# Performance work log

Measured on AMD Instinct MI355X. Metric: run time of the kernel, lower is better.

Reference implementation:

```python
import jax, jax.numpy as jnp
import numpy as np

D_MODEL = 1024
NUM_HEADS = 16
HEAD_DIM = D_MODEL // NUM_HEADS


def setup_inputs() -> dict:
    key = jax.random.key(0)
    k_x, k_wqkv, k_bqkv, k_wfc, k_bfc = jax.random.split(key, 5)
    scale_in = 1.0 / np.sqrt(D_MODEL)
    return {
        "x": jax.random.normal(k_x, (2, 2048, D_MODEL), dtype=jnp.float32),
        # torch nn.Linear stores weight as [out_features, in_features]
        "w_qkv": jax.random.uniform(k_wqkv, (3 * D_MODEL, D_MODEL), jnp.float32, -scale_in, scale_in),
        "b_qkv": jax.random.uniform(k_bqkv, (3 * D_MODEL,), jnp.float32, -scale_in, scale_in),
        "w_fc": jax.random.uniform(k_wfc, (D_MODEL, D_MODEL), jnp.float32, -scale_in, scale_in),
        "b_fc": jax.random.uniform(k_bfc, (D_MODEL,), jnp.float32, -scale_in, scale_in),
    }


def reference(x, w_qkv, b_qkv, w_fc, b_fc):
    B, S, _ = x.shape
    # fused QKV projection: [B,S,3*d_model]
    qkv = jnp.einsum("bsd,ed->bse", x, w_qkv) + b_qkv
    # [B,S,H,3*head_dim] -> [B,H,S,3*head_dim]
    qkv = qkv.reshape(B, S, NUM_HEADS, 3 * HEAD_DIM).transpose(0, 2, 1, 3)
    Q, K, V = jnp.split(qkv, 3, axis=-1)  # each [B,H,S,head_dim]
    scores = jnp.einsum("bhqd,bhkd->bhqk", Q, K) / np.sqrt(HEAD_DIM).astype(np.float32)
    attention = jax.nn.softmax(scores, axis=-1)  # [B,H,S,S]
    values = jnp.einsum("bhqk,bhkd->bhqd", attention, V)
    # [B,H,S,head_dim] -> [B,S,d_model]
    values = values.transpose(0, 2, 1, 3).reshape(B, S, D_MODEL)
    out = jnp.einsum("bsd,ed->bse", values, w_fc) + b_fc
    return out
```

## Files before the change

### kernel.cpp

```cpp
#include <hip/hip_runtime.h>
#include <hip/hip_bf16.h>

#define D_MODEL 1024
#define NH 16
#define HD 64
#define BATCH 2
#define SEQ 2048

typedef __attribute__((ext_vector_type(8))) short short8;
typedef __attribute__((ext_vector_type(4))) float floatx4;

static __device__ __forceinline__ short f2bf(float f) {
    __hip_bfloat16 h = __float2bfloat16(f);
    return *reinterpret_cast<short*>(&h);
}
static __device__ __forceinline__ unsigned int pk2bf(float a, float b) {
    float2 t; t.x = a; t.y = b;
    __hip_bfloat162 h2 = __float22bfloat162_rn(t);
    return *reinterpret_cast<unsigned int*>(&h2);
}

__global__ __launch_bounds__(256) void cvt_all(
    const float* __restrict__ x, const float* __restrict__ wq,
    const float* __restrict__ wf,
    short* __restrict__ Xb, short* __restrict__ Wqb, short* __restrict__ Wfb)
{
    int i = blockIdx.x * 256 + threadIdx.x;
    const float* src; short* dst; int off;
    if (i < 524288)      { src = x;  dst = Xb;  off = i; }
    else if (i < 917504) { src = wq; dst = Wqb; off = i - 524288; }
    else                 { src = wf; dst = Wfb; off = i - 917504; }
    float4 a = *reinterpret_cast<const float4*>(src + off * 8);
    float4 b = *reinterpret_cast<const float4*>(src + off * 8 + 4);
    short8 o;
    o[0] = f2bf(a.x); o[1] = f2bf(a.y); o[2] = f2bf(a.z); o[3] = f2bf(a.w);
    o[4] = f2bf(b.x); o[5] = f2bf(b.y); o[6] = f2bf(b.z); o[7] = f2bf(b.w);
    *reinterpret_cast<short8*>(dst + off * 8) = o;
}

__global__ __launch_bounds__(256) void qkv_gemm(
    const short* __restrict__ X, const short* __restrict__ W,
    const float* __restrict__ bias,
    short* __restrict__ Qs, short* __restrict__ Ks, short* __restrict__ Vt_g)
{
    __shared__ __align__(16) short As[128][72];
    __shared__ __align__(16) short Bs[64][72];
    const int tid = threadIdx.x;
    const int bx = blockIdx.x;
    const int m0 = blockIdx.y * 128;
    const int n0 = bx * 64;
    const int h = bx / 3, t = bx % 3;
    const int bi = m0 >> 11;
    const int sl0 = m0 & 2047;
    const int w = tid >> 6, lane = tid & 63;
    const int quad = lane >> 4, l15 = lane & 15;
    const int wm2 = w >> 1, wn2 = w & 1;

    floatx4 acc[4][2];
#pragma unroll
    for (int i = 0; i < 4; i++)
#pragma unroll
        for (int j = 0; j < 2; j++) acc[i][j] = (floatx4)0.0f;

    for (int k0 = 0; k0 < 1024; k0 += 64) {
        __syncthreads();
#pragma unroll
        for (int i = 0; i < 4; i++) {
            int c = tid + i * 256;
            int row = c >> 3, ck = c & 7;
            *reinterpret_cast<uint4*>(&As[row][ck * 8]) =
                *reinterpret_cast<const uint4*>(&X[(m0 + row) * 1024 + k0 + ck * 8]);
        }
#pragma unroll
        for (int i = 0; i < 2; i++) {
            int c = tid + i * 256;
            int row = c >> 3, ck = c & 7;
            *reinterpret_cast<uint4*>(&Bs[row][ck * 8]) =
                *reinterpret_cast<const uint4*>(&W[(n0 + row) * 1024 + k0 + ck * 8]);
        }
        __syncthreads();
#pragma unroll
        for (int kk = 0; kk < 2; kk++) {
            short8 a[4], b[2];
#pragma unroll
            for (int i = 0; i < 4; i++)
                a[i] = *reinterpret_cast<const short8*>(&As[wm2 * 64 + i * 16 + l15][kk * 32 + quad * 8]);
#pragma unroll
            for (int j = 0; j < 2; j++)
                b[j] = *reinterpret_cast<const short8*>(&Bs[wn2 * 32 + j * 16 + l15][kk * 32 + quad * 8]);
#pragma unroll
            for (int mt = 0; mt < 4; mt++)
#pragma unroll
                for (int nt = 0; nt < 2; nt++)
                    acc[mt][nt] = __builtin_amdgcn_mfma_f32_16x16x32_bf16(
                        a[mt], b[nt], acc[mt][nt], 0, 0, 0);
        }
    }

    __syncthreads();
    short* T = &As[0][0];
#pragma unroll
    for (int nt = 0; nt < 2; nt++) {
        int col = wn2 * 32 + nt * 16 + l15;
        float bv = bias[h * 192 + t * 64 + col];
#pragma unroll
        for (int mt = 0; mt < 4; mt++) {
#pragma unroll
            for (int r = 0; r < 4; r++) {
                int ml = wm2 * 64 + mt * 16 + quad * 4 + r;
                float v = acc[mt][nt][r] + bv;
                if (t == 0) v *= 0.125f;
                if (t < 2) As[ml][col] = f2bf(v);
                else       T[col * 136 + ml] = f2bf(v);
            }
        }
    }
    __syncthreads();

    if (t < 2) {
        short* dst = (t == 0) ? Qs : Ks;
#pragma unroll
        for (int i = 0; i < 4; i++) {
            int c = tid + i * 256;
            int row = c >> 3, ck = c & 7;
            uint4 u = *reinterpret_cast<const uint4*>(&As[row][ck * 8]);
            *reinterpret_cast<uint4*>(
                &dst[((size_t)(bi * NH + h) * SEQ + sl0 + row) * HD + ck * 8]) = u;
        }
    } else {
#pragma unroll
        for (int i = 0; i < 4; i++) {
            int c = tid + i * 256;
            int drow = c >> 4, ck = c & 15;
            uint4 u = *reinterpret_cast<const uint4*>(&T[drow * 136 + ck * 8]);
            *reinterpret_cast<uint4*>(
                &Vt_g[((size_t)(bi * NH + h) * HD + drow) * SEQ + sl0 + ck * 8]) = u;
        }
    }
}

__global__ __launch_bounds__(256) void attn_kernel(
    const short* __restrict__ Qs, const short* __restrict__ Ks,
    const short* __restrict__ Vt_g, short* __restrict__ attn)
{
    __shared__ __align__(16) short Kl[64][72];
    __shared__ __align__(16) short Vt[64][72];
    __shared__ __align__(16) short Pl[4][32][72];
    __shared__ float Ls[128];

    const int tid = threadIdx.x;
    const int w = tid >> 6, lane = tid & 63;
    const int quad = lane >> 4, l15 = lane & 15;
    const int q0 = blockIdx.x * 128;
    const int h = blockIdx.y, bi = blockIdx.z;
    const int bh = bi * NH + h;
    const int kbase = bh * SEQ * HD;
    const int vbase = bh * HD * SEQ;

    short8 aq[2][2];
#pragma unroll
    for (int qt2 = 0; qt2 < 2; qt2++) {
        const short* qp = Qs + kbase + (q0 + w * 32 + qt2 * 16 + l15) * HD;
#pragma unroll
        for (int c = 0; c < 2; c++)
            aq[qt2][c] = *reinterpret_cast<const short8*>(qp + c * 32 + quad * 8);
    }

    float l_acc[2] = {0.f, 0.f};
    floatx4 o[2][4];
#pragma unroll
    for (int mt = 0; mt < 2; mt++)
#pragma unroll
        for (int nt = 0; nt < 4; nt++) o[mt][nt] = (floatx4)0.0f;

    for (int kt = 0; kt < SEQ; kt += 64) {
        __syncthreads();
#pragma unroll
        for (int i = 0; i < 2; i++) {
            int c = tid + i * 256;
            int row = c >> 3, ck = c & 7;
            *reinterpret_cast<uint4*>(&Kl[row][ck * 8]) =
                *reinterpret_cast<const uint4*>(&Ks[kbase + (kt + row) * HD + ck * 8]);
            *reinterpret_cast<uint4*>(&Vt[row][ck * 8]) =
                *reinterpret_cast<const uint4*>(&Vt_g[vbase + row * SEQ + kt + ck * 8]);
        }
        __syncthreads();

        floatx4 sf[4][2];
#pragma unroll
        for (int kt2 = 0; kt2 < 4; kt2++)
#pragma unroll
            for (int qt2 = 0; qt2 < 2; qt2++) sf[kt2][qt2] = (floatx4)0.0f;
#pragma unroll
        for (int c = 0; c < 2; c++) {
#pragma unroll
            for (int kt2 = 0; kt2 < 4; kt2++) {
                short8 bk = *reinterpret_cast<const short8*>(
                    &Kl[kt2 * 16 + l15][c * 32 + quad * 8]);
#pragma unroll
                for (int qt2 = 0; qt2 < 2; qt2++)
                    sf[kt2][qt2] = __builtin_amdgcn_mfma_f32_16x16x32_bf16(
                        bk, aq[qt2][c], sf[kt2][qt2], 0, 0, 0);
            }
        }

#pragma unroll
        for (int kt2 = 0; kt2 < 4; kt2++) {
#pragma unroll
            for (int qt2 = 0; qt2 < 2; qt2++) {
                float e0 = __expf(sf[kt2][qt2][0]);
                float e1 = __expf(sf[kt2][qt2][1]);
                float e2 = __expf(sf[kt2][qt2][2]);
                float e3 = __expf(sf[kt2][qt2][3]);
                l_acc[qt2] += (e0 + e1) + (e2 + e3);
                uint2 p;
                p.x = pk2bf(e0, e1);
                p.y = pk2bf(e2, e3);
                *reinterpret_cast<uint2*>(&Pl[w][qt2 * 16 + l15][kt2 * 16 + quad * 4]) = p;
            }
        }
        asm volatile("s_waitcnt lgkmcnt(0)" ::: "memory");

#pragma unroll
        for (int c = 0; c < 2; c++) {
#pragma unroll
            for (int mt = 0; mt < 2; mt++) {
                short8 ap = *reinterpret_cast<const short8*>(
                    &Pl[w][mt * 16 + l15][c * 32 + quad * 8]);
#pragma unroll
                for (int nt = 0; nt < 4; nt++) {
                    short8 bv = *reinterpret_cast<const short8*>(
                        &Vt[nt * 16 + l15][c * 32 + quad * 8]);
                    o[mt][nt] = __builtin_amdgcn_mfma_f32_16x16x32_bf16(
                        ap, bv, o[mt][nt], 0, 0, 0);
                }
            }
        }
    }

#pragma unroll
    for (int qt2 = 0; qt2 < 2; qt2++) {
        l_acc[qt2] += __shfl_xor(l_acc[qt2], 16);
        l_acc[qt2] += __shfl_xor(l_acc[qt2], 32);
    }
    if (quad == 0) {
        Ls[w * 32 + l15] = l_acc[0];
        Ls[w * 32 + 16 + l15] = l_acc[1];
    }
    asm volatile("s_waitcnt lgkmcnt(0)" ::: "memory");

#pragma unroll
    for (int mt = 0; mt < 2; mt++) {
#pragma unroll
        for (int r = 0; r < 4; r++) {
            int ql = w * 32 + mt * 16 + quad * 4 + r;
            float lt = Ls[ql];
#pragma unroll
            for (int nt = 0; nt < 4; nt++) {
                attn[(bi * SEQ + q0 + ql) * D_MODEL + h * HD + nt * 16 + l15] =
                    f2bf(o[mt][nt][r] / lt);
            }
        }
    }
}

__global__ __launch_bounds__(256) void fc_gemm(
    const short* __restrict__ A, const short* __restrict__ W,
    const float* __restrict__ bias, float* __restrict__ out)
{
    __shared__ __align__(16) short As[128][72];
    __shared__ __align__(16) short Bs[64][72];
    const int tid = threadIdx.x;
    const int m0 = blockIdx.y * 128;
    const int n0 = blockIdx.x * 64;
    const int w = tid >> 6, lane = tid & 63;
    const int quad = lane >> 4, l15 = lane & 15;
    const int wm2 = w >> 1, wn2 = w & 1;

    floatx4 acc[4][2];
#pragma unroll
    for (int i = 0; i < 4; i++)
#pragma unroll
        for (int j = 0; j < 2; j++) acc[i][j] = (floatx4)0.0f;

    for (int k0 = 0; k0 < 1024; k0 += 64) {
        __syncthreads();
#pragma unroll
        for (int i = 0; i < 4; i++) {
            int c = tid + i * 256;
            int row = c >> 3, ck = c & 7;
            *reinterpret_cast<uint4*>(&As[row][ck * 8]) =
                *reinterpret_cast<const uint4*>(&A[(m0 + row) * 1024 + k0 + ck * 8]);
        }
#pragma unroll
        for (int i = 0; i < 2; i++) {
            int c = tid + i * 256;
            int row = c >> 3, ck = c & 7;
            *reinterpret_cast<uint4*>(&Bs[row][ck * 8]) =
                *reinterpret_cast<const uint4*>(&W[(n0 + row) * 1024 + k0 + ck * 8]);
        }
        __syncthreads();
#pragma unroll
        for (int kk = 0; kk < 2; kk++) {
            short8 a[4], b[2];
#pragma unroll
            for (int i = 0; i < 4; i++)
                a[i] = *reinterpret_cast<const short8*>(&As[wm2 * 64 + i * 16 + l15][kk * 32 + quad * 8]);
#pragma unroll
            for (int j = 0; j < 2; j++)
                b[j] = *reinterpret_cast<const short8*>(&Bs[wn2 * 32 + j * 16 + l15][kk * 32 + quad * 8]);
#pragma unroll
            for (int mt = 0; mt < 4; mt++)
#pragma unroll
                for (int nt = 0; nt < 2; nt++)
                    acc[mt][nt] = __builtin_amdgcn_mfma_f32_16x16x32_bf16(
                        a[mt], b[nt], acc[mt][nt], 0, 0, 0);
        }
    }

#pragma unroll
    for (int nt = 0; nt < 2; nt++) {
        int col = n0 + wn2 * 32 + nt * 16 + l15;
        float bv = bias[col];
#pragma unroll
        for (int mt = 0; mt < 4; mt++) {
#pragma unroll
            for (int r = 0; r < 4; r++) {
                int row = m0 + wm2 * 64 + mt * 16 + quad * 4 + r;
                out[row * 1024 + col] = acc[mt][nt][r] + bv;
            }
        }
    }
}

extern "C" void kernel_launch(void* const* d_in, const int* in_sizes, int n_in,
                              void* d_out, int out_size, void* d_ws, size_t ws_size,
                              hipStream_t stream) {
    const float* x     = (const float*)d_in[0];
    const float* w_qkv = (const float*)d_in[1];
    const float* b_qkv = (const float*)d_in[2];
    const float* w_fc  = (const float*)d_in[3];
    const float* b_fc  = (const float*)d_in[4];
    float* out = (float*)d_out;

    const size_t M4 = 4u * 1024 * 1024;
    short* Xb    = (short*)d_ws;
    short* Wqb   = Xb + M4;
    short* Wfb   = Wqb + 3u * 1024 * 1024;
    short* Qs    = Wfb + 1024 * 1024;
    short* Ks    = Qs + M4;
    short* Vt_g  = Ks + M4;
    short* attnb = Xb;

    cvt_all<<<4096, 256, 0, stream>>>(x, w_qkv, w_fc, Xb, Wqb, Wfb);
    qkv_gemm<<<dim3(48, 32), 256, 0, stream>>>(Xb, Wqb, b_qkv, Qs, Ks, Vt_g);
    attn_kernel<<<dim3(16, 16, 2), 256, 0, stream>>>(Qs, Ks, Vt_g, attnb);
    fc_gemm<<<dim3(16, 32), 256, 0, stream>>>(attnb, Wfb, b_fc, out);
}
```

Measured before the change: 222.4 us.

## Load K/V fragments directly to registers with prefetch, remap attention grid, use exp2

The attention kernel no longer stages K and V tiles through shared memory. Each wave loads its MFMA operand fragments straight from global memory into registers and prefetches the next tile during compute, which removes two block barriers per iteration. The Q scale now folds in log2(e) so the kernel can call exp2f instead of __expf. The grid is flattened and remapped so that neighbouring blocks cover different (batch, head) pairs, with the aim of improving L2/XCD locality. The cost is redundant global loads, since all four waves fetch the same K/V, plus higher register pressure.

```diff
diff --git a/kernel.cpp b/kernel.cpp
--- a/kernel.cpp
+++ b/kernel.cpp
@@ -109,7 +109,7 @@
             for (int r = 0; r < 4; r++) {
                 int ml = wm2 * 64 + mt * 16 + quad * 4 + r;
                 float v = acc[mt][nt][r] + bv;
-                if (t == 0) v *= 0.125f;
+                if (t == 0) v *= 0.18033688f;
                 if (t < 2) As[ml][col] = f2bf(v);
                 else       T[col * 136 + ml] = f2bf(v);
             }
@@ -143,17 +143,16 @@
     const short* __restrict__ Qs, const short* __restrict__ Ks,
     const short* __restrict__ Vt_g, short* __restrict__ attn)
 {
-    __shared__ __align__(16) short Kl[64][72];
-    __shared__ __align__(16) short Vt[64][72];
     __shared__ __align__(16) short Pl[4][32][72];
     __shared__ float Ls[128];
 
     const int tid = threadIdx.x;
     const int w = tid >> 6, lane = tid & 63;
     const int quad = lane >> 4, l15 = lane & 15;
-    const int q0 = blockIdx.x * 128;
-    const int h = blockIdx.y, bi = blockIdx.z;
-    const int bh = bi * NH + h;
+    const int j = blockIdx.x;
+    const int bh = (j & 7) * 4 + ((j >> 3) & 3);
+    const int q0 = (j >> 5) * 128;
+    const int bi = bh >> 4, h = bh & 15;
     const int kbase = bh * SEQ * HD;
     const int vbase = bh * HD * SEQ;
 
@@ -166,6 +165,21 @@
             aq[qt2][c] = *reinterpret_cast<const short8*>(qp + c * 32 + quad * 8);
     }
 
+    const short* kp = Ks + kbase + l15 * HD + quad * 8;
+    const short* vp = Vt_g + vbase + l15 * SEQ + quad * 8;
+
+    short8 kf[8], vf[8];
+#pragma unroll
+    for (int kt2 = 0; kt2 < 4; kt2++)
+#pragma unroll
+        for (int c = 0; c < 2; c++)
+            kf[kt2 * 2 + c] = *reinterpret_cast<const short8*>(kp + kt2 * 16 * HD + c * 32);
+#pragma unroll
+    for (int nt = 0; nt < 4; nt++)
+#pragma unroll
+        for (int c = 0; c < 2; c++)
+            vf[nt * 2 + c] = *reinterpret_cast<const short8*>(vp + nt * 16 * SEQ + c * 32);
+
     float l_acc[2] = {0.f, 0.f};
     floatx4 o[2][4];
 #pragma unroll
@@ -174,44 +188,28 @@
         for (int nt = 0; nt < 4; nt++) o[mt][nt] = (floatx4)0.0f;
 
     for (int kt = 0; kt < SEQ; kt += 64) {
-        __syncthreads();
-#pragma unroll
-        for (int i = 0; i < 2; i++) {
-            int c = tid + i * 256;
-            int row = c >> 3, ck = c & 7;
-            *reinterpret_cast<uint4*>(&Kl[row][ck * 8]) =
-                *reinterpret_cast<const uint4*>(&Ks[kbase + (kt + row) * HD + ck * 8]);
-            *reinterpret_cast<uint4*>(&Vt[row][ck * 8]) =
-                *reinterpret_cast<const uint4*>(&Vt_g[vbase + row * SEQ + kt + ck * 8]);
-        }
-        __syncthreads();
-
         floatx4 sf[4][2];
 #pragma unroll
         for (int kt2 = 0; kt2 < 4; kt2++)
 #pragma unroll
             for (int qt2 = 0; qt2 < 2; qt2++) sf[kt2][qt2] = (floatx4)0.0f;
 #pragma unroll
-        for (int c = 0; c < 2; c++) {
-#pragma unroll
-            for (int kt2 = 0; kt2 < 4; kt2++) {
-                short8 bk = *reinterpret_cast<const short8*>(
-                    &Kl[kt2 * 16 + l15][c * 32 + quad * 8]);
+        for (int c = 0; c < 2; c++)
+#pragma unroll
+            for (int kt2 = 0; kt2 < 4; kt2++)
 #pragma unroll
                 for (int qt2 = 0; qt2 < 2; qt2++)
                     sf[kt2][qt2] = __builtin_amdgcn_mfma_f32_16x16x32_bf16(
-                        bk, aq[qt2][c], sf[kt2][qt2], 0, 0, 0);
-            }
-        }
+                        kf[kt2 * 2 + c], aq[qt2][c], sf[kt2][qt2], 0, 0, 0);
 
 #pragma unroll
         for (int kt2 = 0; kt2 < 4; kt2++) {
 #pragma unroll
             for (int qt2 = 0; qt2 < 2; qt2++) {
-                float e0 = __expf(sf[kt2][qt2][0]);
-                float e1 = __expf(sf[kt2][qt2][1]);
-                float e2 = __expf(sf[kt2][qt2][2]);
-                float e3 = __expf(sf[kt2][qt2][3]);
+                float e0 = exp2f(sf[kt2][qt2][0]);
+                float e1 = exp2f(sf[kt2][qt2][1]);
+                float e2 = exp2f(sf[kt2][qt2][2]);
+                float e3 = exp2f(sf[kt2][qt2][3]);
                 l_acc[qt2] += (e0 + e1) + (e2 + e3);
                 uint2 p;
                 p.x = pk2bf(e0, e1);
@@ -221,6 +219,15 @@
         }
         asm volatile("s_waitcnt lgkmcnt(0)" ::: "memory");
 
+        if (kt + 64 < SEQ) {
+            const short* kpn = kp + (kt + 64) * HD;
+#pragma unroll
+            for (int kt2 = 0; kt2 < 4; kt2++)
+#pragma unroll
+                for (int c = 0; c < 2; c++)
+                    kf[kt2 * 2 + c] = *reinterpret_cast<const short8*>(kpn + kt2 * 16 * HD + c * 32);
+        }
+
 #pragma unroll
         for (int c = 0; c < 2; c++) {
 #pragma unroll
@@ -228,13 +235,19 @@
                 short8 ap = *reinterpret_cast<const short8*>(
                     &Pl[w][mt * 16 + l15][c * 32 + quad * 8]);
 #pragma unroll
-                for (int nt = 0; nt < 4; nt++) {
-                    short8 bv = *reinterpret_cast<const short8*>(
-                        &Vt[nt * 16 + l15][c * 32 + quad * 8]);
+                for (int nt = 0; nt < 4; nt++)
                     o[mt][nt] = __builtin_amdgcn_mfma_f32_16x16x32_bf16(
-                        ap, bv, o[mt][nt], 0, 0, 0);
-                }
-            }
+                        ap, vf[nt * 2 + c], o[mt][nt], 0, 0, 0);
+            }
+        }
+
+        if (kt + 64 < SEQ) {
+            const short* vpn = vp + (kt + 64);
+#pragma unroll
+            for (int nt = 0; nt < 4; nt++)
+#pragma unroll
+                for (int c = 0; c < 2; c++)
+                    vf[nt * 2 + c] = *reinterpret_cast<const short8*>(vpn + nt * 16 * SEQ + c * 32);
         }
     }
 
@@ -354,6 +367,6 @@
 
     cvt_all<<<4096, 256, 0, stream>>>(x, w_qkv, w_fc, Xb, Wqb, Wfb);
     qkv_gemm<<<dim3(48, 32), 256, 0, stream>>>(Xb, Wqb, b_qkv, Qs, Ks, Vt_g);
-    attn_kernel<<<dim3(16, 16, 2), 256, 0, stream>>>(Qs, Ks, Vt_g, attnb);
+    attn_kernel<<<512, 256, 0, stream>>>(Qs, Ks, Vt_g, attnb);
     fc_gemm<<<dim3(16, 32), 256, 0, stream>>>(attnb, Wfb, b_fc, out);
 }
```

Measured after the change: 260.4 us. +17.1%, slower.

## Widen QKV GEMM tiles, double-buffer attention K/V, use exp2 softmax

Applied to the files above, without the earlier changes.

The QKV GEMM now computes 128x128 tiles instead of 128x64, so each block writes two head-slices in sequence and A-tile reuse doubles. The attention kernel double-buffers K and V in shared memory, prefetching the next tile into registers during the MFMA work, which removes one barrier per iteration. Q is prescaled by log2(e)/8 so the softmax can use exp2f instead of __expf. The costs are more registers and LDS per block and fewer QKV blocks in the grid.

```diff
diff --git a/kernel.cpp b/kernel.cpp
--- a/kernel.cpp
+++ b/kernel.cpp
@@ -44,23 +44,20 @@
     short* __restrict__ Qs, short* __restrict__ Ks, short* __restrict__ Vt_g)
 {
     __shared__ __align__(16) short As[128][72];
-    __shared__ __align__(16) short Bs[64][72];
+    __shared__ __align__(16) short Bs[128][72];
     const int tid = threadIdx.x;
-    const int bx = blockIdx.x;
     const int m0 = blockIdx.y * 128;
-    const int n0 = bx * 64;
-    const int h = bx / 3, t = bx % 3;
-    const int bi = m0 >> 11;
-    const int sl0 = m0 & 2047;
+    const int n0 = blockIdx.x * 128;
+    const int bi = m0 >> 11, sl0 = m0 & 2047;
     const int w = tid >> 6, lane = tid & 63;
     const int quad = lane >> 4, l15 = lane & 15;
     const int wm2 = w >> 1, wn2 = w & 1;
 
-    floatx4 acc[4][2];
+    floatx4 acc[4][4];
 #pragma unroll
     for (int i = 0; i < 4; i++)
 #pragma unroll
-        for (int j = 0; j < 2; j++) acc[i][j] = (floatx4)0.0f;
+        for (int j = 0; j < 4; j++) acc[i][j] = (floatx4)0.0f;
 
     for (int k0 = 0; k0 < 1024; k0 += 64) {
         __syncthreads();
@@ -70,28 +67,22 @@
             int row = c >> 3, ck = c & 7;
             *reinterpret_cast<uint4*>(&As[row][ck * 8]) =
                 *reinterpret_cast<const uint4*>(&X[(m0 + row) * 1024 + k0 + ck * 8]);
-        }
-#pragma unroll
-        for (int i = 0; i < 2; i++) {
-            int c = tid + i * 256;
-            int row = c >> 3, ck = c & 7;
             *reinterpret_cast<uint4*>(&Bs[row][ck * 8]) =
                 *reinterpret_cast<const uint4*>(&W[(n0 + row) * 1024 + k0 + ck * 8]);
         }
         __syncthreads();
 #pragma unroll
         for (int kk = 0; kk < 2; kk++) {
-            short8 a[4], b[2];
-#pragma unroll
-            for (int i = 0; i < 4; i++)
-                a[i] = *reinterpret_cast<const short8*>(&As[wm2 * 64 + i * 16 + l15][kk * 32 + quad * 8]);
-#pragma unroll
-            for (int j = 0; j < 2; j++)
-                b[j] = *reinterpret_cast<const short8*>(&Bs[wn2 * 32 + j * 16 + l15][kk * 32 + quad * 8]);
+            short8 a[4], b[4];
+#pragma unroll
+            for (int t = 0; t < 4; t++) {
+                a[t] = *reinterpret_cast<const short8*>(&As[wm2 * 64 + t * 16 + l15][kk * 32 + quad * 8]);
+                b[t] = *reinterpret_cast<const short8*>(&Bs[wn2 * 64 + t * 16 + l15][kk * 32 + quad * 8]);
+            }
 #pragma unroll
             for (int mt = 0; mt < 4; mt++)
 #pragma unroll
-                for (int nt = 0; nt < 2; nt++)
+                for (int nt = 0; nt < 4; nt++)
                     acc[mt][nt] = __builtin_amdgcn_mfma_f32_16x16x32_bf16(
                         a[mt], b[nt], acc[mt][nt], 0, 0, 0);
         }
@@ -100,42 +91,50 @@
     __syncthreads();
     short* T = &As[0][0];
 #pragma unroll
-    for (int nt = 0; nt < 2; nt++) {
-        int col = wn2 * 32 + nt * 16 + l15;
-        float bv = bias[h * 192 + t * 64 + col];
-#pragma unroll
-        for (int mt = 0; mt < 4; mt++) {
-#pragma unroll
-            for (int r = 0; r < 4; r++) {
-                int ml = wm2 * 64 + mt * 16 + quad * 4 + r;
-                float v = acc[mt][nt][r] + bv;
-                if (t == 0) v *= 0.125f;
-                if (t < 2) As[ml][col] = f2bf(v);
-                else       T[col * 136 + ml] = f2bf(v);
-            }
-        }
-    }
-    __syncthreads();
-
-    if (t < 2) {
-        short* dst = (t == 0) ? Qs : Ks;
-#pragma unroll
-        for (int i = 0; i < 4; i++) {
-            int c = tid + i * 256;
-            int row = c >> 3, ck = c & 7;
-            uint4 u = *reinterpret_cast<const uint4*>(&As[row][ck * 8]);
-            *reinterpret_cast<uint4*>(
-                &dst[((size_t)(bi * NH + h) * SEQ + sl0 + row) * HD + ck * 8]) = u;
-        }
-    } else {
-#pragma unroll
-        for (int i = 0; i < 4; i++) {
-            int c = tid + i * 256;
-            int drow = c >> 4, ck = c & 15;
-            uint4 u = *reinterpret_cast<const uint4*>(&T[drow * 136 + ck * 8]);
-            *reinterpret_cast<uint4*>(
-                &Vt_g[((size_t)(bi * NH + h) * HD + drow) * SEQ + sl0 + ck * 8]) = u;
-        }
+    for (int half = 0; half < 2; half++) {
+        const int colg0 = n0 + half * 64;
+        const int h = colg0 / 192;
+        const int t = (colg0 % 192) / 64;
+        if (wn2 == half) {
+#pragma unroll
+            for (int nt = 0; nt < 4; nt++) {
+                int jj = nt * 16 + l15;
+                float bv = bias[colg0 + jj];
+#pragma unroll
+                for (int mt = 0; mt < 4; mt++) {
+#pragma unroll
+                    for (int r = 0; r < 4; r++) {
+                        int ml = wm2 * 64 + mt * 16 + quad * 4 + r;
+                        float v = acc[mt][nt][r] + bv;
+                        if (t == 0) v *= 0.18033688f;
+                        if (t < 2) As[ml][jj] = f2bf(v);
+                        else       T[jj * 136 + ml] = f2bf(v);
+                    }
+                }
+            }
+        }
+        __syncthreads();
+        if (t < 2) {
+            short* dst = (t == 0) ? Qs : Ks;
+#pragma unroll
+            for (int i = 0; i < 4; i++) {
+                int c = tid + i * 256;
+                int row = c >> 3, ck = c & 7;
+                uint4 u = *reinterpret_cast<const uint4*>(&As[row][ck * 8]);
+                *reinterpret_cast<uint4*>(
+                    &dst[((size_t)(bi * NH + h) * SEQ + sl0 + row) * HD + ck * 8]) = u;
+            }
+        } else {
+#pragma unroll
+            for (int i = 0; i < 4; i++) {
+                int c = tid + i * 256;
+                int d = c >> 4, ck = c & 15;
+                uint4 u = *reinterpret_cast<const uint4*>(&T[d * 136 + ck * 8]);
+                *reinterpret_cast<uint4*>(
+                    &Vt_g[((size_t)(bi * NH + h) * HD + d) * SEQ + sl0 + ck * 8]) = u;
+            }
+        }
+        __syncthreads();
     }
 }
 
@@ -143,8 +142,8 @@
     const short* __restrict__ Qs, const short* __restrict__ Ks,
     const short* __restrict__ Vt_g, short* __restrict__ attn)
 {
-    __shared__ __align__(16) short Kl[64][72];
-    __shared__ __align__(16) short Vt[64][72];
+    __shared__ __align__(16) short Kl[2][64][72];
+    __shared__ __align__(16) short Vt[2][64][72];
     __shared__ __align__(16) short Pl[4][32][72];
     __shared__ float Ls[128];
 
@@ -157,6 +156,9 @@
     const int kbase = bh * SEQ * HD;
     const int vbase = bh * HD * SEQ;
 
+    const int kr0 = tid >> 3,         kc0 = (tid & 7) * 8;
+    const int kr1 = (tid + 256) >> 3, kc1 = (tid & 7) * 8;
+
     short8 aq[2][2];
 #pragma unroll
     for (int qt2 = 0; qt2 < 2; qt2++) {
@@ -166,6 +168,17 @@
             aq[qt2][c] = *reinterpret_cast<const short8*>(qp + c * 32 + quad * 8);
     }
 
+    {
+        uint4 ka = *reinterpret_cast<const uint4*>(&Ks[kbase + kr0 * HD + kc0]);
+        uint4 kb = *reinterpret_cast<const uint4*>(&Ks[kbase + kr1 * HD + kc1]);
+        uint4 va = *reinterpret_cast<const uint4*>(&Vt_g[vbase + kr0 * SEQ + kc0]);
+        uint4 vb = *reinterpret_cast<const uint4*>(&Vt_g[vbase + kr1 * SEQ + kc1]);
+        *reinterpret_cast<uint4*>(&Kl[0][kr0][kc0]) = ka;
+        *reinterpret_cast<uint4*>(&Kl[0][kr1][kc1]) = kb;
+        *reinterpret_cast<uint4*>(&Vt[0][kr0][kc0]) = va;
+        *reinterpret_cast<uint4*>(&Vt[0][kr1][kc1]) = vb;
+    }
+
     float l_acc[2] = {0.f, 0.f};
     floatx4 o[2][4];
 #pragma unroll
@@ -173,18 +186,19 @@
 #pragma unroll
         for (int nt = 0; nt < 4; nt++) o[mt][nt] = (floatx4)0.0f;
 
-    for (int kt = 0; kt < SEQ; kt += 64) {
-        __syncthreads();
-#pragma unroll
-        for (int i = 0; i < 2; i++) {
-            int c = tid + i * 256;
-            int row = c >> 3, ck = c & 7;
-            *reinterpret_cast<uint4*>(&Kl[row][ck * 8]) =
-                *reinterpret_cast<const uint4*>(&Ks[kbase + (kt + row) * HD + ck * 8]);
-            *reinterpret_cast<uint4*>(&Vt[row][ck * 8]) =
-                *reinterpret_cast<const uint4*>(&Vt_g[vbase + row * SEQ + kt + ck * 8]);
-        }
-        __syncthreads();
+    for (int it = 0; it < SEQ / 64; it++) {
+        const int cur = it & 1;
+        __syncthreads();
+
+        uint4 kna, knb, vna, vnb;
+        const bool more = (it + 1 < SEQ / 64);
+        if (more) {
+            int ktn = (it + 1) * 64;
+            kna = *reinterpret_cast<const uint4*>(&Ks[kbase + (ktn + kr0) * HD + kc0]);
+            knb = *reinterpret_cast<const uint4*>(&Ks[kbase + (ktn + kr1) * HD + kc1]);
+            vna = *reinterpret_cast<const uint4*>(&Vt_g[vbase + kr0 * SEQ + ktn + kc0]);
+            vnb = *reinterpret_cast<const uint4*>(&Vt_g[vbase + kr1 * SEQ + ktn + kc1]);
+        }
 
         floatx4 sf[4][2];
 #pragma unroll
@@ -196,7 +210,7 @@
 #pragma unroll
             for (int kt2 = 0; kt2 < 4; kt2++) {
                 short8 bk = *reinterpret_cast<const short8*>(
-                    &Kl[kt2 * 16 + l15][c * 32 + quad * 8]);
+                    &Kl[cur][kt2 * 16 + l15][c * 32 + quad * 8]);
 #pragma unroll
                 for (int qt2 = 0; qt2 < 2; qt2++)
                     sf[kt2][qt2] = __builtin_amdgcn_mfma_f32_16x16x32_bf16(
@@ -208,10 +222,10 @@
         for (int kt2 = 0; kt2 < 4; kt2++) {
 #pragma unroll
             for (int qt2 = 0; qt2 < 2; qt2++) {
-                float e0 = __expf(sf[kt2][qt2][0]);
-                float e1 = __expf(sf[kt2][qt2][1]);
-                float e2 = __expf(sf[kt2][qt2][2]);
-                float e3 = __expf(sf[kt2][qt2][3]);
+                float e0 = exp2f(sf[kt2][qt2][0]);
+                float e1 = exp2f(sf[kt2][qt2][1]);
+                float e2 = exp2f(sf[kt2][qt2][2]);
+                float e3 = exp2f(sf[kt2][qt2][3]);
                 l_acc[qt2] += (e0 + e1) + (e2 + e3);
                 uint2 p;
                 p.x = pk2bf(e0, e1);
@@ -230,11 +244,19 @@
 #pragma unroll
                 for (int nt = 0; nt < 4; nt++) {
                     short8 bv = *reinterpret_cast<const short8*>(
-                        &Vt[nt * 16 + l15][c * 32 + quad * 8]);
+                        &Vt[cur][nt * 16 + l15][c * 32 + quad * 8]);
                     o[mt][nt] = __builtin_amdgcn_mfma_f32_16x16x32_bf16(
                         ap, bv, o[mt][nt], 0, 0, 0);
                 }
             }
+        }
+
+        if (more) {
+            int nxt = 1 - cur;
+            *reinterpret_cast<uint4*>(&Kl[nxt][kr0][kc0]) = kna;
+            *reinterpret_cast<uint4*>(&Kl[nxt][kr1][kc1]) = knb;
+            *reinterpret_cast<uint4*>(&Vt[nxt][kr0][kc0]) = vna;
+            *reinterpret_cast<uint4*>(&Vt[nxt][kr1][kc1]) = vnb;
         }
     }
 
@@ -353,7 +375,7 @@
     short* attnb = Xb;
 
     cvt_all<<<4096, 256, 0, stream>>>(x, w_qkv, w_fc, Xb, Wqb, Wfb);
-    qkv_gemm<<<dim3(48, 32), 256, 0, stream>>>(Xb, Wqb, b_qkv, Qs, Ks, Vt_g);
+    qkv_gemm<<<dim3(24, 32), 256, 0, stream>>>(Xb, Wqb, b_qkv, Qs, Ks, Vt_g);
     attn_kernel<<<dim3(16, 16, 2), 256, 0, stream>>>(Qs, Ks, Vt_g, attnb);
     fc_gemm<<<dim3(16, 32), 256, 0, stream>>>(attnb, Wfb, b_fc, out);
 }
```

After: 228.9 us. +2.9%, slower.
